# Performance work log

Hardware: AMD Instinct MI355X
Metric: run time of the kernel (lower is better)

The kernel has to match this reference:

```python
import jax, jax.numpy as jnp
import numpy as np

B, N_HEADS, H, W, DIM = 8, 12, 32, 32, 768
HEAD_DIM = DIM // N_HEADS  # 64
N = 1 + H * W  # cls token + spatial tokens


def setup_inputs() -> dict:
    key = jax.random.key(0)
    ks = jax.random.split(key, 8)
    x = jax.random.normal(ks[0], (B, N, DIM), dtype=jnp.float32)
    mask = jax.random.bernoulli(ks[1], 0.7, (B, N))
    mask = mask.at[:, 0].set(True)  # cls token always valid
    qkv_w = jax.random.normal(ks[2], (DIM, 3 * DIM), dtype=jnp.float32) * 0.02
    qkv_b = jnp.zeros((3 * DIM,), dtype=jnp.float32)
    proj_w = jax.random.normal(ks[3], (DIM, DIM), dtype=jnp.float32) * 0.02
    proj_b = jnp.zeros((DIM,), dtype=jnp.float32)
    rel_pos_h = jax.random.normal(ks[4], (2 * H - 1, HEAD_DIM), dtype=jnp.float32) * 0.02
    rel_pos_w = jax.random.normal(ks[5], (2 * W - 1, HEAD_DIM), dtype=jnp.float32) * 0.02
    return {"x": x, "mask": mask, "qkv_w": qkv_w, "qkv_b": qkv_b,
            "proj_w": proj_w, "proj_b": proj_b,
            "rel_pos_h": rel_pos_h, "rel_pos_w": rel_pos_w}


def _rel_pos_bias(q_spatial, rel_pos_h, rel_pos_w):
    # q_spatial: [B, heads, H, W, head_dim]; q_shape == k_shape so ratios are 1
    idx_h = jnp.arange(H)[:, None] - jnp.arange(H)[None, :] + (H - 1)  # [H, H]
    idx_w = jnp.arange(W)[:, None] - jnp.arange(W)[None, :] + (W - 1)  # [W, W]
    Rh = rel_pos_h[idx_h]  # [H, kH, c]
    Rw = rel_pos_w[idx_w]  # [W, kW, c]
    rel_h = jnp.einsum('byhwc,hkc->byhwk', q_spatial, Rh)  # [B,heads,H,W,kH]
    rel_w = jnp.einsum('byhwc,wkc->byhwk', q_spatial, Rw)  # [B,heads,H,W,kW]
    bias = rel_h[..., :, None] + rel_w[..., None, :]        # [B,heads,H,W,kH,kW]
    return bias.reshape(q_spatial.shape[0], q_spatial.shape[1], H * W, H * W)


def reference(x, mask, qkv_w, qkv_b, proj_w, proj_b, rel_pos_h, rel_pos_w):
    scale = HEAD_DIM ** -0.5
    qkv = (x @ qkv_w + qkv_b).reshape(B, N, 3, N_HEADS, HEAD_DIM)
    qkv = jnp.transpose(qkv, (2, 0, 3, 1, 4))
    q, k, v = qkv[0], qkv[1], qkv[2]
    attn = jnp.einsum('bhqd,bhkd->bhqk', q, k) * scale  # [B,heads,N,N]
    # spatial relative position bias on the non-cls block (cal_rel_pos_spatial)
    r_q = q[:, :, 1:, :].reshape(B, N_HEADS, H, W, HEAD_DIM)
    bias = _rel_pos_bias(r_q, rel_pos_h, rel_pos_w)
    attn = attn.at[:, :, 1:, 1:].add(bias)
    # attention mask: outer product of 1D token masks
    m = mask.astype(attn.dtype)
    mask2d = jnp.einsum('bi,bj->bij', m, m)[:, None, :, :]
    attn = attn - 1e9 * (1.0 - mask2d)
    attn = jax.nn.softmax(attn, axis=-1)
    out = jnp.einsum('bhqk,bhkd->bhqd', attn, v)
    out = jnp.transpose(out, (0, 2, 1, 3)).reshape(B, N, DIM)
    out = out @ proj_w + proj_b
    # GlobalMaxPoolLayer with use_class_token=True: masked GAP + max over spatial tokens
    x_sp = out[:, 1:, :]
    m_sp = mask[:, 1:].astype(jnp.float32)[..., None]
    avg = jnp.sum(x_sp * m_sp, axis=1, keepdims=True) / (jnp.sum(m_sp, axis=1, keepdims=True) + 1e-7)
    mx = jnp.max(x_sp, axis=1, keepdims=True)
    pooled = jnp.concatenate([avg, mx], axis=-1)  # [B, 1, 2*DIM]
    return pooled
```

## Files before the change

### kernel.cpp

```cpp
#include <hip/hip_runtime.h>
#include <hip/hip_bf16.h>

typedef __attribute__((ext_vector_type(8))) short short8v;
typedef __attribute__((ext_vector_type(4))) float f32x4;
typedef __attribute__((ext_vector_type(16))) float f32x16;

constexpr int B_  = 8;
constexpr int NH  = 12;
constexpr int DIM = 768;
constexpr int HD  = 64;
constexpr int N_  = 1025;
constexpr int NSP = 1024;
constexpr int K3  = 2304;
constexpr int VT  = 34;

constexpr size_t KV_BYTES = (size_t)B_*NH*VT*4096;

constexpr size_t OFF_MASK  = 0;
constexpr size_t OFF_PC    = 49152;
constexpr size_t OFF_QKVWT = 65536;
constexpr size_t OFF_PROJWT= OFF_QKVWT + (size_t)K3*768*2;
constexpr size_t OFF_Q     = OFF_PROJWT + (size_t)768*768*2;
constexpr size_t OFF_K     = OFF_Q + (size_t)B_*NH*N_*HD*2;
constexpr size_t OFF_V     = OFF_K + KV_BYTES;
constexpr size_t OFF_AO    = OFF_V + KV_BYTES;
constexpr size_t OFF_PS    = OFF_AO + (size_t)8192*768*2;
constexpr size_t OFF_PM    = OFF_PS + 64*768*4;
constexpr size_t OFF_XB    = OFF_PM + 64*768*4;

__device__ inline float b2f(unsigned short u) {
  union { unsigned int ui; float f; } x; x.ui = ((unsigned int)u) << 16; return x.f;
}
__device__ inline unsigned short f2b(float f) {
  union { float f; unsigned int u; } x; x.f = f;
  unsigned int r = x.u + 0x7FFFu + ((x.u >> 16) & 1u);
  return (unsigned short)(r >> 16);
}
__device__ inline unsigned int cvtpk(float lo, float hi) {
  unsigned int r;
  asm("v_cvt_pk_bf16_f32 %0, %1, %2" : "=v"(r) : "v"(lo), "v"(hi));
  return r;
}
__device__ inline short8v pack8(float4 lo, float4 hi) {
  union { unsigned int u[4]; short8v s; } r;
  r.u[0] = cvtpk(lo.x, lo.y); r.u[1] = cvtpk(lo.z, lo.w);
  r.u[2] = cvtpk(hi.x, hi.y); r.u[3] = cvtpk(hi.z, hi.w);
  return r.s;
}
__device__ inline float fexp2(float x) {
  float r;
  asm("v_exp_f32 %0, %1" : "=v"(r) : "v"(x));
  return r;
}
__device__ inline void plswap(unsigned int& a, unsigned int& b) {
  asm("v_permlane32_swap_b32 %0, %1" : "+v"(a), "+v"(b));
}
__device__ inline void gload16(const void* g, void* l) {
  __builtin_amdgcn_global_load_lds(
      (const __attribute__((address_space(1))) void*)g,
      (__attribute__((address_space(3))) void*)l, 16, 0, 0);
}
template<int NWG>
__device__ inline int xcd_swz(int bid) {
  constexpr int q = NWG / 8, r = NWG % 8;
  const int x = bid & 7, i = bid >> 3;
  return (x < r ? x * (q + 1) : r * (q + 1) + (x - r) * q) + i;
}

__global__ __launch_bounds__(256) void preproc(
    const unsigned char* __restrict__ mraw, float* __restrict__ mask_f,
    float* __restrict__ pcnt, unsigned short* __restrict__ kW,
    unsigned short* __restrict__ vW,
    const float* __restrict__ qkv_w, const float* __restrict__ proj_w,
    unsigned short* __restrict__ qkvwT, unsigned short* __restrict__ projwT,
    const float* __restrict__ x, unsigned short* __restrict__ xb)
{
  const int g = blockIdx.x, t = threadIdx.x;
  if (g < 96) {
    unsigned short* kz = kW + ((size_t)g * VT + 32) * 2048;
    for (int i = t; i < 2048; i += 256) kz[i] = 0;
    unsigned short* vz = vW + ((size_t)g * VT + 32) * 2048;
    for (int i = t; i < 2048; i += 256) vz[i] = 0;
    return;
  }
  if (g == 96) {
    __shared__ int flags[2];
    __shared__ float cnt8[8];
    if (t < 2) flags[t] = 0;
    if (t < 8) cnt8[t] = 0.f;
    __syncthreads();
    const int n = B_ * N_;
    int f1 = 0, f0 = 0;
    for (int i = t; i < n; i += 256) {
      unsigned char vv = mraw[i];
      if (vv) { int m = i & 3; if (m == 1) f1 = 1; if (m == 0) f0 = 1; }
    }
    if (f1) atomicOr(&flags[0], 1);
    if (f0) atomicOr(&flags[1], 1);
    __syncthreads();
    const bool isBool = flags[0] != 0;
    const bool isInt  = !isBool && (flags[1] != 0);
    for (int i = t; i < n; i += 256) {
      float v;
      if (isBool)     v = mraw[i] ? 1.f : 0.f;
      else if (isInt) v = ((const int*)mraw)[i] ? 1.f : 0.f;
      else            v = ((const float*)mraw)[i];
      mask_f[i] = v;
      const int b = i / 1025, nn = i - b * 1025;
      if (nn > 0) atomicAdd(&cnt8[b], v);
    }
    __syncthreads();
    if (t < 8) pcnt[t] = cnt8[t];
    return;
  }
  if (g < 2401) {
    __shared__ float tile[32][33];
    const float* in; unsigned short* out; int N, bx, by;
    if (g < 1825) { const int idx = g - 97;  in = qkv_w;  out = qkvwT;  N = K3;  bx = idx % 72; by = idx / 72; }
    else          { const int idx = g - 1825; in = proj_w; out = projwT; N = 768; bx = idx % 24; by = idx / 24; }
    const int tx = t & 31, ty0 = t >> 5;
    const int n0 = bx * 32, k0 = by * 32;
#pragma unroll
    for (int i = 0; i < 4; ++i) {
      const int r = ty0 + i * 8;
      tile[r][tx] = in[(size_t)(k0 + r) * N + n0 + tx];
    }
    __syncthreads();
#pragma unroll
    for (int i = 0; i < 4; ++i) {
      const int r = ty0 + i * 8;
      out[(size_t)(n0 + r) * 768 + k0 + tx] = f2b(tile[tx][r]);
    }
    return;
  }
  const int idx = g - 2401;
  const int n4 = 8200 * 768 / 4;
  for (int i = idx * 256 + t; i < n4; i += 2048 * 256) {
    float4 v = *(const float4*)&x[i * 4];
    ushort4 u;
    u.x = f2b(v.x); u.y = f2b(v.y); u.z = f2b(v.z); u.w = f2b(v.w);
    *(ushort4*)&xb[i * 4] = u;
  }
}

template<int MODE, int GX, int NWG>
__global__ __launch_bounds__(256) void gemm_bf16(
    const unsigned short* __restrict__ A, const unsigned short* __restrict__ BT,
    const float* __restrict__ bias,
    unsigned short* __restrict__ qo, unsigned short* __restrict__ ko,
    unsigned short* __restrict__ vo,
    const float* __restrict__ mask_f, float* __restrict__ psum,
    float* __restrict__ pmax, int M)
{
  __shared__ unsigned short As[2][128 * 32];
  __shared__ unsigned short Bs[2][128 * 32];
  __shared__ float Ms[128];
  const int t = threadIdx.x;
  const int l = t & 63, w = t >> 6;
  const int lg16 = l >> 4, lm16 = l & 15;
  const int wr = w >> 1, wc = w & 1;
  const int wg = xcd_swz<NWG>(blockIdx.x);
  const int by = wg / GX, bx = wg - by * GX;
  const int m0 = by * 128, n0 = bx * 128;

  if (MODE == 1 && t < 128) {
    const int b0 = m0 >> 10, nr = m0 & 1023;
    Ms[t] = mask_f[b0 * N_ + 1 + nr + t];
  }

  f32x4 acc[4][4];
#pragma unroll
  for (int i = 0; i < 4; ++i)
#pragma unroll
    for (int j = 0; j < 4; ++j) acc[i][j] = (f32x4){0.f, 0.f, 0.f, 0.f};

  const int row0 = t >> 2, qq = (t & 3) * 8;
  const unsigned short* Asrc0 = A + (size_t)(m0 + row0) * 768 + qq;
  const unsigned short* Asrc1 = A + (size_t)(m0 + row0 + 64) * 768 + qq;
  const unsigned short* Bsrc0 = BT + (size_t)(n0 + row0) * 768 + qq;
  const unsigned short* Bsrc1 = BT + (size_t)(n0 + row0 + 64) * 768 + qq;

#define STAGE(bi, k0)                                                    \
  do {                                                                   \
    gload16(Asrc0 + (k0), (char*)&As[bi][0] + w * 1024);                 \
    gload16(Asrc1 + (k0), (char*)&As[bi][0] + 4096 + w * 1024);          \
    gload16(Bsrc0 + (k0), (char*)&Bs[bi][0] + w * 1024);                 \
    gload16(Bsrc1 + (k0), (char*)&Bs[bi][0] + 4096 + w * 1024);          \
  } while (0)

  STAGE(0, 0);

#pragma unroll
  for (int kk = 0; kk < 24; ++kk) {
    const int cur = kk & 1;
    if (kk < 23) {
      STAGE(cur ^ 1, (kk + 1) * 32);
      asm volatile("s_waitcnt vmcnt(4)" ::: "memory");
    } else {
      asm volatile("s_waitcnt vmcnt(0)" ::: "memory");
    }
    asm volatile("s_barrier" ::: "memory");
    short8v af[4], bf4[4];
#pragma unroll
    for (int mi = 0; mi < 4; ++mi)
      af[mi] = *(const short8v*)&As[cur][(wr * 64 + mi * 16 + lm16) * 32 + lg16 * 8];
#pragma unroll
    for (int ni = 0; ni < 4; ++ni)
      bf4[ni] = *(const short8v*)&Bs[cur][(wc * 64 + ni * 16 + lm16) * 32 + lg16 * 8];
#pragma unroll
    for (int mi = 0; mi < 4; ++mi)
#pragma unroll
      for (int ni = 0; ni < 4; ++ni)
        acc[mi][ni] = __builtin_amdgcn_mfma_f32_16x16x32_bf16(
            af[mi], bf4[ni], acc[mi][ni], 0, 0, 0);
    asm volatile("s_barrier" ::: "memory");
  }
#undef STAGE

  if (MODE == 1) {
    __syncthreads();
    float* sred = (float*)&As[0][0];
    float* xred = sred + 256;
#pragma unroll
    for (int ni = 0; ni < 4; ++ni) {
      const int cidx = wc * 64 + ni * 16 + lm16;
      const float bv = bias[n0 + cidx];
      float s = 0.f, xm = -3.402823466e+38f;
#pragma unroll
      for (int mi = 0; mi < 4; ++mi)
#pragma unroll
        for (int r = 0; r < 4; ++r) {
          const float v = acc[mi][ni][r] + bv;
          const float m = Ms[wr * 64 + mi * 16 + lg16 * 4 + r];
          s = fmaf(v, m, s);
          xm = fmaxf(xm, v);
        }
      s += __shfl_xor(s, 16);
      s += __shfl_xor(s, 32);
      xm = fmaxf(xm, __shfl_xor(xm, 16));
      xm = fmaxf(xm, __shfl_xor(xm, 32));
      if (lg16 == 0) {
        sred[wr * 128 + cidx] = s;
        xred[wr * 128 + cidx] = xm;
      }
    }
    __syncthreads();
    if (t < 128) {
      const float s  = sred[t] + sred[128 + t];
      const float xm = fmaxf(xred[t], xred[128 + t]);
      psum[(size_t)by * 768 + n0 + t] = s;
      pmax[(size_t)by * 768 + n0 + t] = xm;
    }
  } else {
#pragma unroll
    for (int mi = 0; mi < 4; ++mi) {
      const int r0 = m0 + wr * 64 + mi * 16 + lg16 * 4;
#pragma unroll
      for (int ni = 0; ni < 4; ++ni) {
        const int col = n0 + wc * 64 + ni * 16 + lm16;
        const int which = col / 768;
        const int rem = col - which * 768;
        const int head = rem >> 6, d = rem & 63;
        const float bv = bias[col];
#pragma unroll
        for (int r = 0; r < 4; ++r) {
          const int grow = r0 + r;
          if (grow >= M) continue;
          const int b = grow / 1025;
          const int n = grow - b * 1025;
          const unsigned short val = f2b(acc[mi][ni][r] + bv);
          const int bh = b * NH + head;
          if (which == 0) {
            qo[((size_t)bh * N_ + n) * HD + d] = val;
          } else if (which == 1) {
            ko[((size_t)bh * VT + (n >> 5)) * 2048 + (d >> 4) * 512 +
               ((((d >> 3) & 1) << 5) + (n & 31)) * 8 + (d & 7)] = val;
          } else {
            const int kvloc = n & 31;
            vo[((size_t)bh * VT + (n >> 5)) * 2048 +
               ((d >> 5) * 2 + (kvloc >> 4)) * 512 +
               ((((kvloc >> 3) & 1) << 5) + (d & 31)) * 8 + (kvloc & 7)] = val;
          }
        }
      }
    }
  }
}

__global__ __launch_bounds__(256, 3) void attn_mfma(
    const unsigned short* __restrict__ qp, const unsigned short* __restrict__ kp,
    const unsigned short* __restrict__ vp, const float* __restrict__ mask_f,
    const float* __restrict__ rph, const float* __restrict__ rpw,
    unsigned short* __restrict__ ao)
{
  const int bid = blockIdx.x;
  const int xcd = bid & 7, wx = bid >> 3;
  const int qblk = wx / 12, hl = wx - qblk * 12;
  const int bh = xcd * 12 + hl;
  const int b = bh / NH, head = bh - b * NH;

  const int t = threadIdx.x, w = t >> 6, lane = t & 63;
  const int qi = lane & 31, h = lane >> 5;
  const int row = w * 32 + qi;
  constexpr float L2E = 1.44269504f;
  constexpr float SCL = 0.125f * L2E;
  constexpr float MCOL = -1.44269504e9f;
  constexpr float THR_L = 5.77f;

  __shared__ __align__(16) float bh_lds[128][34];
  __shared__ __align__(16) float ct_lds[1088];
  __shared__ __align__(16) unsigned short T16[128][64];
  float* ctm = (float*)&T16[0][0];

  const unsigned short* qbp = qp + (size_t)bh * N_ * HD;
  const unsigned short* kbp = kp + (size_t)bh * VT * 2048;
  const unsigned short* vbp = vp + (size_t)bh * VT * 2048;
  const int qw0 = qblk * 128 + w * 32;
  const int q = qw0 + qi;

  for (int i = t; i < 1088; i += 256)
    ct_lds[i] = (i < N_) ? (MCOL * (1.f - mask_f[b * N_ + i])) : -2e30f;

  short8v qf[4];
#pragma unroll
  for (int c = 0; c < 4; ++c)
    qf[c] = *(const short8v*)&qbp[(size_t)(1 + q) * HD + c * 16 + h * 8];

  {
    const int hq = q >> 5;
    f32x16 sbh = {}, sb1 = {}, sb2 = {};
    const float* rh0 = rph + (size_t)(hq + 31 - qi) * HD + h * 8;
    const float* rw1 = rpw + (size_t)qi * HD + h * 8;
    const float* rw2 = rpw + (size_t)(qi < 31 ? 32 + qi : 62) * HD + h * 8;
#pragma unroll
    for (int c = 0; c < 4; ++c) {
      short8v a1 = pack8(*(const float4*)(rh0 + c * 16), *(const float4*)(rh0 + c * 16 + 4));
      sbh = __builtin_amdgcn_mfma_f32_32x32x16_bf16(a1, qf[c], sbh, 0, 0, 0);
      short8v a2 = pack8(*(const float4*)(rw1 + c * 16), *(const float4*)(rw1 + c * 16 + 4));
      sb1 = __builtin_amdgcn_mfma_f32_32x32x16_bf16(a2, qf[c], sb1, 0, 0, 0);
      short8v a3 = pack8(*(const float4*)(rw2 + c * 16), *(const float4*)(rw2 + c * 16 + 4));
      sb2 = __builtin_amdgcn_mfma_f32_32x32x16_bf16(a3, qf[c], sb2, 0, 0, 0);
    }
#pragma unroll
    for (int r = 0; r < 16; ++r) {
      const int kh = (r & 3) + 8 * (r >> 2) + 4 * h;
      bh_lds[row][kh]   = sbh[r] * L2E;
      T16[row][kh]      = f2b(sb1[r] * L2E);
      T16[row][kh + 32] = f2b(sb2[r] * L2E);
    }
    if (h == 0) { bh_lds[row][32] = 0.f; bh_lds[row][33] = 0.f; }
  }
  __syncthreads();

  float bwv[16];
#pragma unroll
  for (int r = 0; r < 16; ++r) {
    const int kvS = (r & 3) + 8 * (r >> 2) + 4 * h;
    const int kw = (kvS + 31) & 31;
    bwv[r] = b2f(T16[row][qi - kw + 31]);
  }
  __syncthreads();
  for (int i = t; i < 1088; i += 256)
    ctm[i] = (i <= 1024) ? MCOL : -2e30f;
  __syncthreads();

  const float mi_s = mask_f[b * N_ + 1 + q];
  const bool mzero = (mi_s == 0.f);
  const float* ctp = mzero ? ctm : ct_lds;
  const float h0sel = (h == 0) ? 1.f : 0.f;
  float m_lm = -1e30f, l_lane = 0.f;
  float bh_prev = -bwv[0];
  f32x16 oaccA = {}, oaccB = {};

  const char* kptr = (const char*)kbp + lane * 16;
  const char* vptr = (const char*)vbp + lane * 16;

  short8v kf[4];
#pragma unroll
  for (int c = 0; c < 4; ++c) kf[c] = *(const short8v*)(kptr + c * 1024);
  kptr += 4096;
  f32x16 sP = {}, sQ = {};
  sP = __builtin_amdgcn_mfma_f32_32x32x16_bf16(kf[0], qf[0], sP, 0, 0, 0);
  sP = __builtin_amdgcn_mfma_f32_32x32x16_bf16(kf[1], qf[1], sP, 0, 0, 0);
  sP = __builtin_amdgcn_mfma_f32_32x32x16_bf16(kf[2], qf[2], sP, 0, 0, 0);
  sP = __builtin_amdgcn_mfma_f32_32x32x16_bf16(kf[3], qf[3], sP, 0, 0, 0);

#define AITER(KT, SC, SN, DOPREF)                                            \
  do {                                                                       \
    short8v vf00 = *(const short8v*)(vptr);                                  \
    short8v vf01 = *(const short8v*)(vptr + 1024);                           \
    short8v vf10 = *(const short8v*)(vptr + 2048);                           \
    short8v vf11 = *(const short8v*)(vptr + 3072);                           \
    vptr += 4096;                                                            \
    if (DOPREF) {                                                            \
      kf[0] = *(const short8v*)(kptr);                                       \
      kf[1] = *(const short8v*)(kptr + 1024);                                \
      kf[2] = *(const short8v*)(kptr + 2048);                                \
      kf[3] = *(const short8v*)(kptr + 3072);                                \
      kptr += 4096;                                                          \
    }                                                                        \
    const float bh_k = bh_lds[row][KT];                                      \
    const float bh_use = mzero ? 0.f : bh_k;                                 \
    f32x4 ct4[4];                                                            \
    ct4[0] = *(const f32x4*)&ctp[(KT) * 32 + h * 4];                         \
    ct4[1] = *(const f32x4*)&ctp[(KT) * 32 + 8 + h * 4];                     \
    ct4[2] = *(const f32x4*)&ctp[(KT) * 32 + 16 + h * 4];                    \
    ct4[3] = *(const f32x4*)&ctp[(KT) * 32 + 24 + h * 4];                    \
    float lgp[16];                                                           \
    _Pragma("unroll")                                                        \
    for (int r = 0; r < 16; ++r)                                             \
      lgp[r] = fmaf(SCL, SC[r], bwv[r] + ct4[r >> 2][r & 3]);                \
    lgp[0] = fmaf(h0sel, bh_prev - bh_use, lgp[0]);                          \
    bh_prev = bh_k;                                                          \
    float a0 = fmaxf(lgp[0], lgp[1]),  a1 = fmaxf(lgp[2], lgp[3]);           \
    float a2 = fmaxf(lgp[4], lgp[5]),  a3 = fmaxf(lgp[6], lgp[7]);           \
    float a4 = fmaxf(lgp[8], lgp[9]),  a5 = fmaxf(lgp[10], lgp[11]);         \
    float a6 = fmaxf(lgp[12], lgp[13]), a7 = fmaxf(lgp[14], lgp[15]);        \
    float tm = fmaxf(fmaxf(fmaxf(a0, a1), fmaxf(a2, a3)),                    \
                     fmaxf(fmaxf(a4, a5), fmaxf(a6, a7)));                   \
    tm = fmaxf(tm, __shfl_xor(tm, 32));                                      \
    const float tmT = tm + bh_use;                                           \
    if (__any(tmT > m_lm + THR_L)) {                                         \
      const float nm = fmaxf(m_lm, tmT);                                     \
      const float rf = fexp2(m_lm - nm);                                     \
      m_lm = nm; l_lane *= rf;                                               \
      _Pragma("unroll")                                                      \
      for (int r = 0; r < 16; ++r) { oaccA[r] *= rf; oaccB[r] *= rf; }       \
    }                                                                        \
    const float mm = bh_use - m_lm;                                          \
    float p[16];                                                             \
    _Pragma("unroll")                                                        \
    for (int r = 0; r < 16; ++r) p[r] = fexp2(lgp[r] + mm);                  \
    l_lane += (((p[0]+p[1])+(p[2]+p[3]))+((p[4]+p[5])+(p[6]+p[7])))          \
            + (((p[8]+p[9])+(p[10]+p[11]))+((p[12]+p[13])+(p[14]+p[15])));   \
    unsigned int x0 = cvtpk(p[0], p[1]),  x1 = cvtpk(p[2], p[3]);            \
    unsigned int z0 = cvtpk(p[4], p[5]),  z1 = cvtpk(p[6], p[7]);            \
    plswap(x0, z0); plswap(x1, z1);                                          \
    unsigned int y0 = cvtpk(p[8], p[9]),  y1 = cvtpk(p[10], p[11]);          \
    unsigned int w0_ = cvtpk(p[12], p[13]), w1_ = cvtpk(p[14], p[15]);       \
    plswap(y0, w0_); plswap(y1, w1_);                                        \
    union { unsigned int u[4]; short8v v; } uf1, uf2;                        \
    uf1.u[0] = x0; uf1.u[1] = x1; uf1.u[2] = z0; uf1.u[3] = z1;              \
    uf2.u[0] = y0; uf2.u[1] = y1; uf2.u[2] = w0_; uf2.u[3] = w1_;            \
    if (DOPREF) {                                                            \
      f32x16 sn = {};                                                        \
      sn = __builtin_amdgcn_mfma_f32_32x32x16_bf16(kf[0], qf[0], sn, 0, 0, 0); \
      sn = __builtin_amdgcn_mfma_f32_32x32x16_bf16(kf[1], qf[1], sn, 0, 0, 0); \
      sn = __builtin_amdgcn_mfma_f32_32x32x16_bf16(kf[2], qf[2], sn, 0, 0, 0); \
      sn = __builtin_amdgcn_mfma_f32_32x32x16_bf16(kf[3], qf[3], sn, 0, 0, 0); \
      SN = sn;                                                               \
    }                                                                        \
    oaccA = __builtin_amdgcn_mfma_f32_32x32x16_bf16(vf00, uf1.v, oaccA, 0, 0, 0); \
    oaccA = __builtin_amdgcn_mfma_f32_32x32x16_bf16(vf01, uf2.v, oaccA, 0, 0, 0); \
    oaccB = __builtin_amdgcn_mfma_f32_32x32x16_bf16(vf10, uf1.v, oaccB, 0, 0, 0); \
    oaccB = __builtin_amdgcn_mfma_f32_32x32x16_bf16(vf11, uf2.v, oaccB, 0, 0, 0); \
  } while (0)

  for (int kt2 = 0; kt2 < 16; ++kt2) {
    AITER(2 * kt2,     sP, sQ, true);
    AITER(2 * kt2 + 1, sQ, sP, true);
  }
  AITER(32, sP, sQ, false);
#undef AITER

  __syncthreads();

  const float l_tot = l_lane + __shfl_xor(l_lane, 32);
  const float inv = 1.f / l_tot;
  char* tbase = (char*)&T16[0][0] + row * 128;
  const int rsw = (row & 7) << 4;
#pragma unroll
  for (int r = 0; r < 16; r += 2) {
    const int d = (r & 3) + 8 * (r >> 2) + 4 * h;
    const unsigned int uA = cvtpk(oaccA[r] * inv, oaccA[r + 1] * inv);
    const unsigned int uB = cvtpk(oaccB[r] * inv, oaccB[r + 1] * inv);
    const int bo1 = 2 * d, bo2 = 2 * d + 64;
    *(unsigned int*)(tbase + (((bo1 & ~15) ^ rsw) | (bo1 & 15))) = uA;
    *(unsigned int*)(tbase + (((bo2 & ~15) ^ rsw) | (bo2 & 15))) = uB;
  }
  const int q2 = lane >> 1, hb = lane & 1;
  const int srow = w * 32 + q2;
  const char* sbase = (const char*)&T16[0][0] + srow * 128;
  const int ssw = srow & 7;
  unsigned short* dst =
      ao + (size_t)(b * NSP + qw0 + q2) * DIM + head * HD + hb * 32;
#pragma unroll
  for (int i = 0; i < 4; ++i) {
    const int ci = hb * 4 + i;
    short8v v = *(const short8v*)(sbase + ((ci ^ ssw) << 4));
    *(short8v*)(dst + i * 8) = v;
  }
}

__global__ __launch_bounds__(256) void pool_stage2(
    const float* __restrict__ psum, const float* __restrict__ pmax,
    const float* __restrict__ pcnt, float* __restrict__ out)
{
  const int b = blockIdx.y;
  const int c = blockIdx.x * 256 + threadIdx.x;
  float s = 0.f, mx = -3.402823466e+38f;
#pragma unroll
  for (int z = 0; z < 8; ++z) {
    s  += psum[(size_t)(b * 8 + z) * 768 + c];
    mx  = fmaxf(mx, pmax[(size_t)(b * 8 + z) * 768 + c]);
  }
  const float cnt = pcnt[b];
  out[b * 1536 + c]       = s / (cnt + 1e-7f);
  out[b * 1536 + 768 + c] = mx;
}

extern "C" void kernel_launch(void* const* d_in, const int* in_sizes, int n_in,
                              void* d_out, int out_size, void* d_ws, size_t ws_size,
                              hipStream_t stream) {
  const float* x      = (const float*)d_in[0];
  const unsigned char* mraw = (const unsigned char*)d_in[1];
  const float* qkv_w  = (const float*)d_in[2];
  const float* qkv_b  = (const float*)d_in[3];
  const float* proj_w = (const float*)d_in[4];
  const float* proj_b = (const float*)d_in[5];
  const float* rph    = (const float*)d_in[6];
  const float* rpw    = (const float*)d_in[7];

  char* ws = (char*)d_ws;
  float*          mask_f = (float*)(ws + OFF_MASK);
  float*          pcnt   = (float*)(ws + OFF_PC);
  unsigned short* qkvwT  = (unsigned short*)(ws + OFF_QKVWT);
  unsigned short* projwT = (unsigned short*)(ws + OFF_PROJWT);
  unsigned short* qW     = (unsigned short*)(ws + OFF_Q);
  unsigned short* kW     = (unsigned short*)(ws + OFF_K);
  unsigned short* vW     = (unsigned short*)(ws + OFF_V);
  unsigned short* aoW    = (unsigned short*)(ws + OFF_AO);
  float*          psum   = (float*)(ws + OFF_PS);
  float*          pmax   = (float*)(ws + OFF_PM);
  unsigned short* xb     = (unsigned short*)(ws + OFF_XB);

  preproc<<<4449, 256, 0, stream>>>(mraw, mask_f, pcnt, kW, vW,
                                    qkv_w, proj_w, qkvwT, projwT, x, xb);

  gemm_bf16<0, 18, 1170><<<1170, 256, 0, stream>>>(
      xb, qkvwT, qkv_b, qW, kW, vW, nullptr, nullptr, nullptr, 8200);

  attn_mfma<<<768, 256, 0, stream>>>(qW, kW, vW, mask_f, rph, rpw, aoW);

  gemm_bf16<1, 6, 384><<<384, 256, 0, stream>>>(
      aoW, projwT, proj_b, nullptr, nullptr, nullptr,
      mask_f, psum, pmax, 8192);

  pool_stage2<<<dim3(3, B_), 256, 0, stream>>>(psum, pmax, pcnt, (float*)d_out);
}
```

Measured before the change: 163.9 us.

## Double-buffer V fragments across attention iterations and raise MFMA wave priority

V tile fragments are now loaded one iteration ahead into ping-pong register buffers, so the global-load latency of V overlaps the previous tile's softmax and MFMA work. The change also wraps the QK and PV MFMA groups in s_setprio so waves issuing matrix ops get scheduler priority. Separately, the QKV-projection epilogue replaces a per-element integer divide by 1025 with one divide per row group plus a conditional wrap. The cost is extra VGPRs for the second V buffer, which could lower occupancy.

```diff
diff --git a/kernel.cpp b/kernel.cpp
--- a/kernel.cpp
+++ b/kernel.cpp
@@ -255,6 +255,8 @@
 #pragma unroll
     for (int mi = 0; mi < 4; ++mi) {
       const int r0 = m0 + wr * 64 + mi * 16 + lg16 * 4;
+      const int b0d = r0 / 1025;
+      const int n0d = r0 - b0d * 1025;
 #pragma unroll
       for (int ni = 0; ni < 4; ++ni) {
         const int col = n0 + wc * 64 + ni * 16 + lm16;
@@ -266,8 +268,8 @@
         for (int r = 0; r < 4; ++r) {
           const int grow = r0 + r;
           if (grow >= M) continue;
-          const int b = grow / 1025;
-          const int n = grow - b * 1025;
+          int b = b0d, n = n0d + r;
+          if (n >= 1025) { b += 1; n -= 1025; }
           const unsigned short val = f2b(acc[mi][ni][r] + bv);
           const int bh = b * NH + head;
           if (which == 0) {
@@ -375,24 +377,27 @@
   const char* kptr = (const char*)kbp + lane * 16;
   const char* vptr = (const char*)vbp + lane * 16;
 
-  short8v kf[4];
+  short8v kf[4], vfA[4], vfB[4];
 #pragma unroll
   for (int c = 0; c < 4; ++c) kf[c] = *(const short8v*)(kptr + c * 1024);
   kptr += 4096;
+#pragma unroll
+  for (int c = 0; c < 4; ++c) vfA[c] = *(const short8v*)(vptr + c * 1024);
+  vptr += 4096;
   f32x16 sP = {}, sQ = {};
   sP = __builtin_amdgcn_mfma_f32_32x32x16_bf16(kf[0], qf[0], sP, 0, 0, 0);
   sP = __builtin_amdgcn_mfma_f32_32x32x16_bf16(kf[1], qf[1], sP, 0, 0, 0);
   sP = __builtin_amdgcn_mfma_f32_32x32x16_bf16(kf[2], qf[2], sP, 0, 0, 0);
   sP = __builtin_amdgcn_mfma_f32_32x32x16_bf16(kf[3], qf[3], sP, 0, 0, 0);
 
-#define AITER(KT, SC, SN, DOPREF)                                            \
+#define AITER(KT, SC, SN, VC, VN, DOPREF)                                    \
   do {                                                                       \
-    short8v vf00 = *(const short8v*)(vptr);                                  \
-    short8v vf01 = *(const short8v*)(vptr + 1024);                           \
-    short8v vf10 = *(const short8v*)(vptr + 2048);                           \
-    short8v vf11 = *(const short8v*)(vptr + 3072);                           \
-    vptr += 4096;                                                            \
     if (DOPREF) {                                                            \
+      VN[0] = *(const short8v*)(vptr);                                       \
+      VN[1] = *(const short8v*)(vptr + 1024);                                \
+      VN[2] = *(const short8v*)(vptr + 2048);                                \
+      VN[3] = *(const short8v*)(vptr + 3072);                                \
+      vptr += 4096;                                                          \
       kf[0] = *(const short8v*)(kptr);                                       \
       kf[1] = *(const short8v*)(kptr + 1024);                                \
       kf[2] = *(const short8v*)(kptr + 2048);                                \
@@ -444,23 +449,27 @@
     uf2.u[0] = y0; uf2.u[1] = y1; uf2.u[2] = w0_; uf2.u[3] = w1_;            \
     if (DOPREF) {                                                            \
       f32x16 sn = {};                                                        \
+      __builtin_amdgcn_s_setprio(1);                                         \
       sn = __builtin_amdgcn_mfma_f32_32x32x16_bf16(kf[0], qf[0], sn, 0, 0, 0); \
       sn = __builtin_amdgcn_mfma_f32_32x32x16_bf16(kf[1], qf[1], sn, 0, 0, 0); \
       sn = __builtin_amdgcn_mfma_f32_32x32x16_bf16(kf[2], qf[2], sn, 0, 0, 0); \
       sn = __builtin_amdgcn_mfma_f32_32x32x16_bf16(kf[3], qf[3], sn, 0, 0, 0); \
+      __builtin_amdgcn_s_setprio(0);                                         \
       SN = sn;                                                               \
     }                                                                        \
-    oaccA = __builtin_amdgcn_mfma_f32_32x32x16_bf16(vf00, uf1.v, oaccA, 0, 0, 0); \
-    oaccA = __builtin_amdgcn_mfma_f32_32x32x16_bf16(vf01, uf2.v, oaccA, 0, 0, 0); \
-    oaccB = __builtin_amdgcn_mfma_f32_32x32x16_bf16(vf10, uf1.v, oaccB, 0, 0, 0); \
-    oaccB = __builtin_amdgcn_mfma_f32_32x32x16_bf16(vf11, uf2.v, oaccB, 0, 0, 0); \
+    __builtin_amdgcn_s_setprio(1);                                           \
+    oaccA = __builtin_amdgcn_mfma_f32_32x32x16_bf16(VC[0], uf1.v, oaccA, 0, 0, 0); \
+    oaccA = __builtin_amdgcn_mfma_f32_32x32x16_bf16(VC[1], uf2.v, oaccA, 0, 0, 0); \
+    oaccB = __builtin_amdgcn_mfma_f32_32x32x16_bf16(VC[2], uf1.v, oaccB, 0, 0, 0); \
+    oaccB = __builtin_amdgcn_mfma_f32_32x32x16_bf16(VC[3], uf2.v, oaccB, 0, 0, 0); \
+    __builtin_amdgcn_s_setprio(0);                                           \
   } while (0)
 
   for (int kt2 = 0; kt2 < 16; ++kt2) {
-    AITER(2 * kt2,     sP, sQ, true);
-    AITER(2 * kt2 + 1, sQ, sP, true);
-  }
-  AITER(32, sP, sQ, false);
+    AITER(2 * kt2,     sP, sQ, vfA, vfB, true);
+    AITER(2 * kt2 + 1, sQ, sP, vfB, vfA, true);
+  }
+  AITER(32, sP, sQ, vfA, vfB, false);
 #undef AITER
 
   __syncthreads();
```

New measurement: 200.6 us. +22.4%, slower.
